# Kernel tuning notes

Hardware: AMD Instinct MI355X
Metric: run time of the kernel (lower is better)

The kernel has to match this reference:

```python
import jax, jax.numpy as jnp
import numpy as np

B, N, M = 8, 4096, 2048
IN_DIM, D, CTX_DIM = 512, 512, 768


def setup_inputs() -> dict:
    key = jax.random.key(0)
    k_h, k_hr, k_c, k_a, k_k, k_v, k_o = jax.random.split(key, 7)
    s = 0.02  # init scale for weights
    return {
        "h": jax.random.normal(k_h, (B, N, IN_DIM), dtype=jnp.float32),
        "h_retrieved": jax.random.normal(k_hr, (B, M, CTX_DIM), dtype=jnp.float32),
        # torch nn.Linear convention: weight is [out_features, in_features]
        "W_cond": jax.random.normal(k_c, (IN_DIM, CTX_DIM), dtype=jnp.float32) * s,
        "W_attn": jax.random.normal(k_a, (D, IN_DIM), dtype=jnp.float32) * s,
        "W_k": jax.random.normal(k_k, (D, IN_DIM), dtype=jnp.float32) * s,
        "W_v": jax.random.normal(k_v, (D, IN_DIM), dtype=jnp.float32) * s,
        "W_out": jax.random.normal(k_o, (IN_DIM, D), dtype=jnp.float32) * s,
    }


def reference(h, h_retrieved, W_cond, W_attn, W_k, W_v, W_out):
    # cond_flag is True since context_dim != in_dim
    hr = h_retrieved @ W_cond.T                      # [B, M, in_dim]
    attn = jax.nn.softmax(h @ W_attn.T, axis=-1)     # [B, N, d], softmax over channel dim
    kv_in = jnp.concatenate([h, hr], axis=1)         # [B, N+M, in_dim]
    k = kv_in @ W_k.T                                # [B, N+M, d]
    v = kv_in @ W_v.T                                # [B, N+M, d]
    f = jnp.einsum('bnd,bne->bde', k, v)             # K^T V: [B, d, d]
    h_aug = jnp.einsum('bnd,bde->bne', attn, f)      # [B, N, d]
    return h + h_aug @ W_out.T                       # [B, N, in_dim]
```

## Files before the change

### kernel.cpp

```cpp
#include <hip/hip_runtime.h>
#include <hip/hip_bf16.h>


typedef unsigned short u16;
typedef __bf16 bf16x8 __attribute__((ext_vector_type(8)));
typedef float  f32x4  __attribute__((ext_vector_type(4)));
typedef float  f32v4  __attribute__((ext_vector_type(4)));
typedef u16    u16v4  __attribute__((ext_vector_type(4)));
typedef u16    u16v8  __attribute__((ext_vector_type(8)));

__device__ __forceinline__ u16 f2bf(float f) {
  unsigned u = __builtin_bit_cast(unsigned, f);
  u = u + 0x7FFFu + ((u >> 16) & 1u);
  return (u16)(u >> 16);
}
__device__ __forceinline__ float bf2f(u16 s) {
  return __builtin_bit_cast(float, (unsigned)s << 16);
}

__global__ __launch_bounds__(256) void cvt_T(const float* __restrict__ src,
                                             u16* __restrict__ dstT,
                                             long src_bs, long dstT_bs) {
  __shared__ u16 tile[64][72];
  long bz = blockIdx.z;
  const float* S = src + bz * src_bs;
  u16* DT = dstT + bz * dstT_bs;
  int r0 = blockIdx.x * 64;
  int c0 = blockIdx.y * 64;
  int t  = threadIdx.x;
  int tr = t >> 2;
  int tc = (t & 3) * 16;
  const float* sp = &S[(long)(r0 + tr) * 512 + c0 + tc];
#pragma unroll
  for (int q = 0; q < 2; ++q) {
    f32v4 a = *(const f32v4*)(sp + q * 8);
    f32v4 b = *(const f32v4*)(sp + q * 8 + 4);
    u16v8 o;
    o[0] = f2bf(a[0]); o[1] = f2bf(a[1]); o[2] = f2bf(a[2]); o[3] = f2bf(a[3]);
    o[4] = f2bf(b[0]); o[5] = f2bf(b[1]); o[6] = f2bf(b[2]); o[7] = f2bf(b[3]);
    *(u16v8*)&tile[tr][tc + q * 8] = o;
  }
  __syncthreads();
  int tr2 = t >> 3;
  int tc2 = (t & 7) * 8;
#pragma unroll
  for (int it = 0; it < 2; ++it) {
    int cr = it * 32 + tr2;
    u16v8 o;
#pragma unroll
    for (int j = 0; j < 8; ++j) o[j] = tile[tc2 + j][cr];
    *(u16v8*)&DT[(long)(c0 + cr) * 6144 + r0 + tc2] = o;
  }
}

__global__ __launch_bounds__(256) void prep_weights(
    const float* __restrict__ Wc, const float* __restrict__ Wa,
    const float* __restrict__ Wk, const float* __restrict__ Wv,
    const float* __restrict__ Wo,
    u16* __restrict__ wc, u16* __restrict__ wa, u16* __restrict__ wk,
    u16* __restrict__ wv, u16* __restrict__ wvT, u16* __restrict__ wo) {
  __shared__ u16 tile[64][72];
  int bx = blockIdx.x;
  int t = threadIdx.x;
  if (bx < 576) {
    const float* src; u16* dst; long base;
    if (bx < 192)      { src = Wc; dst = wc; base = (long)bx * 2048; }
    else if (bx < 320) { src = Wa; dst = wa; base = (long)(bx - 192) * 2048; }
    else if (bx < 448) { src = Wk; dst = wk; base = (long)(bx - 320) * 2048; }
    else               { src = Wo; dst = wo; base = (long)(bx - 448) * 2048; }
    long i = base + (long)t * 8;
    f32v4 a = *(const f32v4*)(src + i);
    f32v4 b = *(const f32v4*)(src + i + 4);
    u16v8 o;
    o[0] = f2bf(a[0]); o[1] = f2bf(a[1]); o[2] = f2bf(a[2]); o[3] = f2bf(a[3]);
    o[4] = f2bf(b[0]); o[5] = f2bf(b[1]); o[6] = f2bf(b[2]); o[7] = f2bf(b[3]);
    *(u16v8*)(dst + i) = o;
  } else {
    int b2 = bx - 576;
    int r0 = (b2 >> 3) * 64, c0 = (b2 & 7) * 64;
    int tr = t >> 2, tc = (t & 3) * 16;
    const float* sp = &Wv[(long)(r0 + tr) * 512 + c0 + tc];
#pragma unroll
    for (int q = 0; q < 2; ++q) {
      f32v4 a = *(const f32v4*)(sp + q * 8);
      f32v4 b = *(const f32v4*)(sp + q * 8 + 4);
      u16v8 o;
      o[0] = f2bf(a[0]); o[1] = f2bf(a[1]); o[2] = f2bf(a[2]); o[3] = f2bf(a[3]);
      o[4] = f2bf(b[0]); o[5] = f2bf(b[1]); o[6] = f2bf(b[2]); o[7] = f2bf(b[3]);
      *(u16v8*)&wv[(long)(r0 + tr) * 512 + c0 + tc + q * 8] = o;
      *(u16v8*)&tile[tr][tc + q * 8] = o;
    }
    __syncthreads();
    int tr2 = t >> 3, tc2 = (t & 7) * 8;
#pragma unroll
    for (int it = 0; it < 2; ++it) {
      int cr = it * 32 + tr2;
      u16v8 o;
#pragma unroll
      for (int j = 0; j < 8; ++j) o[j] = tile[tc2 + j][cr];
      *(u16v8*)&wvT[(long)(c0 + cr) * 512 + r0 + tc2] = o;
    }
  }
}

__global__ __launch_bounds__(256) void reduce8_bf16(const u16* __restrict__ parts,
                                                    u16* __restrict__ out) {
  long i = (((long)blockIdx.x * 256) + threadIdx.x) * 8;
  long b = i >> 18;
  long r = i & 262143;
  const u16* p = parts + b * 2097152 + r;
  float acc[8] = {};
#pragma unroll
  for (int s = 0; s < 8; ++s) {
    u16v8 v = *(const u16v8*)(p + (long)s * 262144);
#pragma unroll
    for (int j = 0; j < 8; ++j) acc[j] += bf2f(v[j]);
  }
  u16v8 o;
#pragma unroll
  for (int j = 0; j < 8; ++j) o[j] = f2bf(acc[j]);
  *(u16v8*)(out + i) = o;
}

template <int MODE, bool AF32>
__global__ __launch_bounds__(256) void gemm_nt(
    const void* __restrict__ Ap, const u16* __restrict__ B, void* __restrict__ Cout,
    const float* __restrict__ Res, int K, int lda, int ldb, int ldc,
    long sA, long sB, long sC, long sS, long sRes, int kslices) {
  __shared__ __align__(16) char smem_c[65536];

  int gx = gridDim.x, gy = gridDim.y;
  int nwg = gx * gy * (int)gridDim.z;
  int flat = blockIdx.x + gx * (blockIdx.y + gy * blockIdx.z);
  if ((nwg & 7) == 0) { int q = nwg >> 3; flat = (flat & 7) * q + (flat >> 3); }
  int bx = flat % gx; int tmp = flat / gx; int by = tmp % gy; int z = tmp / gy;

  int b = z / kslices;
  int s = z - b * kslices;

  int mt = bx, nt = by;
  if constexpr (MODE == 4) {
    if (bx < 4)      { mt = 0; nt = bx; }
    else if (bx < 7) { mt = 1; nt = bx - 3; }
    else if (bx < 9) { mt = 2; nt = bx - 5; }
    else             { mt = 3; nt = 3; }
  }
  long m0 = (long)mt * 128;
  long n0 = (long)nt * 128;

  const u16* Ag = (const u16*)Ap + (long)b * sA + (long)s * K;
  const float* Af = (const float*)Ap + (long)b * sA;
  const u16* Bg = B + (long)b * sB + (long)s * K;

  int tid  = threadIdx.x;
  int lane = tid & 63;
  int wid  = tid >> 6;
  int wm = wid >> 1, wn = wid & 1;

  int srow = wid * 8 + (lane >> 3);
  int scol = (lane & 7) * 8;
  int arow  = tid >> 1;
  int acolb = (tid & 1) * 32;

  auto stageA = [&](u16* Asd, int k0) {
#pragma unroll
    for (int c = 0; c < 4; ++c) {
      int row = c * 32 + srow;
      __builtin_amdgcn_global_load_lds(
          (const __attribute__((address_space(1))) void*)(Ag + (m0 + row) * lda + k0 + scol),
          (__attribute__((address_space(3))) void*)(Asd + (c * 32 + wid * 8) * 64),
          16, 0, 0);
    }
  };
  auto stageB = [&](u16* Bsd, int k0) {
#pragma unroll
    for (int c = 0; c < 4; ++c) {
      int row = c * 32 + srow;
      __builtin_amdgcn_global_load_lds(
          (const __attribute__((address_space(1))) void*)(Bg + (n0 + row) * ldb + k0 + scol),
          (__attribute__((address_space(3))) void*)(Bsd + (c * 32 + wid * 8) * 64),
          16, 0, 0);
    }
  };
  f32v4 xr[8];
  auto loadA = [&](int k0) {
    const float* sp = Af + (m0 + arow) * (long)lda + k0 + acolb;
#pragma unroll
    for (int q = 0; q < 8; ++q) xr[q] = *(const f32v4*)(sp + q * 4);
  };
  auto cvtA = [&](u16* Asd) {
#pragma unroll
    for (int q = 0; q < 4; ++q) {
      u16v8 o;
      o[0] = f2bf(xr[2*q][0]); o[1] = f2bf(xr[2*q][1]);
      o[2] = f2bf(xr[2*q][2]); o[3] = f2bf(xr[2*q][3]);
      o[4] = f2bf(xr[2*q+1][0]); o[5] = f2bf(xr[2*q+1][1]);
      o[6] = f2bf(xr[2*q+1][2]); o[7] = f2bf(xr[2*q+1][3]);
      *(u16v8*)&Asd[arow * 64 + acolb + q * 8] = o;
    }
  };

  f32x4 acc[4][4] = {};
  int nk = K >> 6;

  if constexpr (AF32) {
    loadA(0);
    cvtA((u16*)smem_c);
    asm volatile("s_waitcnt lgkmcnt(0)" ::: "memory");
  } else {
    stageA((u16*)smem_c, 0);
  }
  stageB((u16*)(smem_c + 32768), 0);

  for (int t = 0; t < nk; ++t) {
    u16* Asc = (u16*)(smem_c + (t & 1) * 16384);
    u16* Bsc = (u16*)(smem_c + 32768 + (t & 1) * 16384);
    u16* Asn = (u16*)(smem_c + ((t + 1) & 1) * 16384);
    u16* Bsn = (u16*)(smem_c + 32768 + ((t + 1) & 1) * 16384);
    bool more = (t + 1) < nk;
    if (more) {
      if constexpr (AF32) {
        loadA((t + 1) * 64);
        stageB(Bsn, (t + 1) * 64);
        asm volatile("s_waitcnt vmcnt(12)\n\ts_barrier" ::: "memory");
      } else {
        stageA(Asn, (t + 1) * 64);
        stageB(Bsn, (t + 1) * 64);
        asm volatile("s_waitcnt vmcnt(8)\n\ts_barrier" ::: "memory");
      }
    } else {
      asm volatile("s_waitcnt vmcnt(0)\n\ts_barrier" ::: "memory");
    }
#pragma unroll
    for (int kk = 0; kk < 2; ++kk) {
      int kofs = kk * 32 + (lane >> 4) * 8;
      bf16x8 af[4], bfr[4];
#pragma unroll
      for (int i = 0; i < 4; ++i) {
        af[i]  = *(const bf16x8*)&Asc[(wm * 64 + i * 16 + (lane & 15)) * 64 + kofs];
        bfr[i] = *(const bf16x8*)&Bsc[(wn * 64 + i * 16 + (lane & 15)) * 64 + kofs];
      }
#pragma unroll
      for (int i = 0; i < 4; ++i)
#pragma unroll
        for (int j = 0; j < 4; ++j)
          acc[i][j] = __builtin_amdgcn_mfma_f32_16x16x32_bf16(af[i], bfr[j], acc[i][j], 0, 0, 0);
    }
    if constexpr (AF32) {
      if (more) cvtA(Asn);
      asm volatile("s_waitcnt lgkmcnt(0)\n\ts_barrier" ::: "memory");
    } else {
      asm volatile("s_barrier" ::: "memory");
    }
  }

  long cb = (long)b * sC + (long)s * sS;
  int lq = lane >> 4;
  int lr = lane & 15;

  if constexpr (MODE == 0 || MODE == 1 || MODE == 4) {
    float* ep = (float*)(smem_c + wid * 4608);
    int row0 = (int)m0 + wm * 64;
    int colb = (int)n0 + wn * 64;
#pragma unroll
    for (int i = 0; i < 4; ++i) {
#pragma unroll
      for (int j = 0; j < 4; ++j)
#pragma unroll
        for (int r = 0; r < 4; ++r)
          ep[(lq * 4 + r) * 72 + lr + j * 16] = acc[i][j][r];
#pragma unroll
      for (int p = 0; p < 4; ++p) {
        int rl = p * 4 + lq;
        f32x4 v = *(f32x4*)&ep[rl * 72 + lr * 4];
        long off = (long)(row0 + i * 16 + rl) * ldc + colb + lr * 4;
        if (MODE == 0 || MODE == 4) {
          u16v4 o;
#pragma unroll
          for (int t2 = 0; t2 < 4; ++t2) o[t2] = f2bf(v[t2]);
          *(u16v4*)((u16*)Cout + cb + off) = o;
        } else {
          const float* R = Res + (long)b * sRes;
          f32v4 rv = *(const f32v4*)&R[off];
          f32v4 ov;
#pragma unroll
          for (int t2 = 0; t2 < 4; ++t2) ov[t2] = v[t2] + rv[t2];
          *(f32v4*)((float*)Cout + cb + off) = ov;
        }
      }
    }
    if constexpr (MODE == 4) {
      if (mt != nt) {
        u16* tT = (u16*)(smem_c + 18432);
#pragma unroll
        for (int i = 0; i < 4; ++i)
#pragma unroll
          for (int j = 0; j < 4; ++j)
#pragma unroll
            for (int r = 0; r < 4; ++r)
              tT[(wn * 64 + j * 16 + lr) * 136 + wm * 64 + i * 16 + lq * 4 + r] =
                  f2bf(acc[i][j][r]);
        __syncthreads();
        int ct   = tid >> 1;
        int half = (tid & 1) * 64;
        u16* dst = (u16*)Cout + cb + (long)(n0 + ct) * ldc + m0 + half;
        const u16* srcl = &tT[ct * 136 + half];
#pragma unroll
        for (int q = 0; q < 8; ++q)
          *(u16v8*)(dst + q * 8) = *(const u16v8*)(srcl + q * 8);
      }
    }
  } else {
    u16* tT = (u16*)smem_c;
#pragma unroll
    for (int i = 0; i < 4; ++i)
#pragma unroll
      for (int j = 0; j < 4; ++j)
#pragma unroll
        for (int r = 0; r < 4; ++r)
          tT[(wn * 64 + j * 16 + lr) * 136 + wm * 64 + i * 16 + lq * 4 + r] =
              f2bf(acc[i][j][r]);
    __syncthreads();
    int ct   = tid >> 1;
    int half = (tid & 1) * 64;
    u16* dst = (u16*)Cout + cb + (long)(n0 + ct) * ldc + m0 + half;
    const u16* srcl = &tT[ct * 136 + half];
#pragma unroll
    for (int q = 0; q < 8; ++q)
      *(u16v8*)(dst + q * 8) = *(const u16v8*)(srcl + q * 8);
  }
}

__global__ __launch_bounds__(256) void gemm64(
    const u16* __restrict__ A, const u16* __restrict__ B, u16* __restrict__ Cout,
    int K, int lda, int ldb, int ldc, long sA, long sB, long sC) {
  __shared__ __align__(16) char smem_c[49152];

  int gx = gridDim.x, gy = gridDim.y;
  int nwg = gx * gy * (int)gridDim.z;
  int flat = blockIdx.x + gx * (blockIdx.y + gy * blockIdx.z);
  if ((nwg & 7) == 0) { int q = nwg >> 3; flat = (flat & 7) * q + (flat >> 3); }
  int bx = flat % gx; int tmp = flat / gx; int by = tmp % gy; int b = tmp / gy;

  long n0 = (long)bx * 128;
  long m0 = (long)by * 64;
  const u16* Ag = A + (long)b * sA;
  const u16* Bg = B + (long)b * sB;

  int tid  = threadIdx.x;
  int lane = tid & 63;
  int wid  = tid >> 6;
  int wm = wid >> 1, wn = wid & 1;

  int srow = wid * 8 + (lane >> 3);
  int scol = (lane & 7) * 8;

  auto stageA = [&](u16* Asd, int k0) {
#pragma unroll
    for (int c = 0; c < 2; ++c) {
      int row = c * 32 + srow;
      __builtin_amdgcn_global_load_lds(
          (const __attribute__((address_space(1))) void*)(Ag + (m0 + row) * lda + k0 + scol),
          (__attribute__((address_space(3))) void*)(Asd + (c * 32 + wid * 8) * 64),
          16, 0, 0);
    }
  };
  auto stageB = [&](u16* Bsd, int k0) {
#pragma unroll
    for (int c = 0; c < 4; ++c) {
      int row = c * 32 + srow;
      __builtin_amdgcn_global_load_lds(
          (const __attribute__((address_space(1))) void*)(Bg + (n0 + row) * ldb + k0 + scol),
          (__attribute__((address_space(3))) void*)(Bsd + (c * 32 + wid * 8) * 64),
          16, 0, 0);
    }
  };

  f32x4 acc[2][4] = {};
  int nk = K >> 6;

  stageA((u16*)smem_c, 0);
  stageB((u16*)(smem_c + 16384), 0);

  for (int t = 0; t < nk; ++t) {
    u16* Asc = (u16*)(smem_c + (t & 1) * 8192);
    u16* Bsc = (u16*)(smem_c + 16384 + (t & 1) * 16384);
    u16* Asn = (u16*)(smem_c + ((t + 1) & 1) * 8192);
    u16* Bsn = (u16*)(smem_c + 16384 + ((t + 1) & 1) * 16384);
    bool more = (t + 1) < nk;
    if (more) {
      stageA(Asn, (t + 1) * 64);
      stageB(Bsn, (t + 1) * 64);
      asm volatile("s_waitcnt vmcnt(6)\n\ts_barrier" ::: "memory");
    } else {
      asm volatile("s_waitcnt vmcnt(0)\n\ts_barrier" ::: "memory");
    }
#pragma unroll
    for (int kk = 0; kk < 2; ++kk) {
      int kofs = kk * 32 + (lane >> 4) * 8;
      bf16x8 af[2], bfr[4];
#pragma unroll
      for (int i = 0; i < 2; ++i)
        af[i]  = *(const bf16x8*)&Asc[(wm * 32 + i * 16 + (lane & 15)) * 64 + kofs];
#pragma unroll
      for (int j = 0; j < 4; ++j)
        bfr[j] = *(const bf16x8*)&Bsc[(wn * 64 + j * 16 + (lane & 15)) * 64 + kofs];
#pragma unroll
      for (int i = 0; i < 2; ++i)
#pragma unroll
        for (int j = 0; j < 4; ++j)
          acc[i][j] = __builtin_amdgcn_mfma_f32_16x16x32_bf16(af[i], bfr[j], acc[i][j], 0, 0, 0);
    }
    asm volatile("s_barrier" ::: "memory");
  }

  int lq = lane >> 4;
  int lr = lane & 15;
  float* ep = (float*)(smem_c + wid * 4608);
  long cb  = (long)b * sC;
  int row0 = (int)m0 + wm * 32;
  int colb = (int)n0 + wn * 64;
#pragma unroll
  for (int i = 0; i < 2; ++i) {
#pragma unroll
    for (int j = 0; j < 4; ++j)
#pragma unroll
      for (int r = 0; r < 4; ++r)
        ep[(lq * 4 + r) * 72 + lr + j * 16] = acc[i][j][r];
#pragma unroll
    for (int p = 0; p < 4; ++p) {
      int rl = p * 4 + lq;
      f32x4 v = *(f32x4*)&ep[rl * 72 + lr * 4];
      long off = (long)(row0 + i * 16 + rl) * ldc + colb + lr * 4;
      u16v4 o;
#pragma unroll
      for (int t2 = 0; t2 < 4; ++t2) o[t2] = f2bf(v[t2]);
      *(u16v4*)(Cout + cb + off) = o;
    }
  }
}

__global__ __launch_bounds__(256, 2) void gemm_sm(
    const float* __restrict__ A,
    const u16* __restrict__ Bw,
    u16* __restrict__ C) {
  __shared__ __align__(16) char smem[73728];
  u16* As = (u16*)smem;
  u16* Bs = (u16*)(smem + 8192);

  int nwg = gridDim.x;
  int flat = blockIdx.x;
  if ((nwg & 7) == 0) { int q = nwg >> 3; flat = (flat & 7) * q + (flat >> 3); }
  long m0 = (long)flat * 64;

  int tid = threadIdx.x;
  int lane = tid & 63;
  int wid = tid >> 6;

  int srow = wid * 8 + (lane >> 3);
  int scol = (lane & 7) * 8;
  int arow  = tid >> 2;
  int acolb = (tid & 3) * 16;

  f32x4 acc[4][8] = {};

  for (int k0 = 0; k0 < 512; k0 += 64) {
    const float* sp = A + (m0 + arow) * 512 + k0 + acolb;
    f32v4 x0 = *(const f32v4*)sp;
    f32v4 x1 = *(const f32v4*)(sp + 4);
    f32v4 x2 = *(const f32v4*)(sp + 8);
    f32v4 x3 = *(const f32v4*)(sp + 12);
#pragma unroll
    for (int c = 0; c < 16; ++c) {
      int row = c * 32 + srow;
      __builtin_amdgcn_global_load_lds(
          (const __attribute__((address_space(1))) void*)(Bw + (long)row * 512 + k0 + scol),
          (__attribute__((address_space(3))) void*)(Bs + (c * 32 + wid * 8) * 64),
          16, 0, 0);
    }
    u16v8 o0, o1;
    o0[0] = f2bf(x0[0]); o0[1] = f2bf(x0[1]); o0[2] = f2bf(x0[2]); o0[3] = f2bf(x0[3]);
    o0[4] = f2bf(x1[0]); o0[5] = f2bf(x1[1]); o0[6] = f2bf(x1[2]); o0[7] = f2bf(x1[3]);
    o1[0] = f2bf(x2[0]); o1[1] = f2bf(x2[1]); o1[2] = f2bf(x2[2]); o1[3] = f2bf(x2[3]);
    o1[4] = f2bf(x3[0]); o1[5] = f2bf(x3[1]); o1[6] = f2bf(x3[2]); o1[7] = f2bf(x3[3]);
    *(u16v8*)&As[arow * 64 + acolb] = o0;
    *(u16v8*)&As[arow * 64 + acolb + 8] = o1;
    __syncthreads();
#pragma unroll
    for (int kk = 0; kk < 2; ++kk) {
      int kofs = kk * 32 + (lane >> 4) * 8;
      bf16x8 af[4], bfr[8];
#pragma unroll
      for (int i = 0; i < 4; ++i)
        af[i] = *(const bf16x8*)&As[(i * 16 + (lane & 15)) * 64 + kofs];
#pragma unroll
      for (int j = 0; j < 8; ++j)
        bfr[j] = *(const bf16x8*)&Bs[(wid * 128 + j * 16 + (lane & 15)) * 64 + kofs];
#pragma unroll
      for (int i = 0; i < 4; ++i)
#pragma unroll
        for (int j = 0; j < 8; ++j)
          acc[i][j] = __builtin_amdgcn_mfma_f32_16x16x32_bf16(af[i], bfr[j], acc[i][j], 0, 0, 0);
    }
    __syncthreads();
  }

  int lq = lane >> 4, lr = lane & 15;
  float* sm = (float*)smem;
  float* ss = (float*)(smem + 1024);

#pragma unroll
  for (int i = 0; i < 4; ++i)
#pragma unroll
    for (int r = 0; r < 4; ++r) {
      float m = acc[i][0][r];
#pragma unroll
      for (int j = 1; j < 8; ++j) m = fmaxf(m, acc[i][j][r]);
#pragma unroll
      for (int o = 1; o < 16; o <<= 1) m = fmaxf(m, __shfl_xor(m, o, 16));
      if (lr == 0) sm[(i * 16 + lq * 4 + r) * 4 + wid] = m;
    }
  __syncthreads();
  float rinv[4][4];
#pragma unroll
  for (int i = 0; i < 4; ++i)
#pragma unroll
    for (int r = 0; r < 4; ++r) {
      f32v4 g4 = *(const f32v4*)&sm[(i * 16 + lq * 4 + r) * 4];
      float gm = fmaxf(fmaxf(g4[0], g4[1]), fmaxf(g4[2], g4[3]));
      float s = 0.f;
#pragma unroll
      for (int j = 0; j < 8; ++j) {
        float e = __expf(acc[i][j][r] - gm);
        acc[i][j][r] = e;
        s += e;
      }
#pragma unroll
      for (int o = 1; o < 16; o <<= 1) s += __shfl_xor(s, o, 16);
      if (lr == 0) ss[(i * 16 + lq * 4 + r) * 4 + wid] = s;
    }
  __syncthreads();
#pragma unroll
  for (int i = 0; i < 4; ++i)
#pragma unroll
    for (int r = 0; r < 4; ++r) {
      f32v4 g4 = *(const f32v4*)&ss[(i * 16 + lq * 4 + r) * 4];
      rinv[i][r] = 1.0f / (g4[0] + g4[1] + g4[2] + g4[3]);
    }
  __syncthreads();

  float* ep = (float*)(smem + wid * 4608);
#pragma unroll
  for (int i = 0; i < 4; ++i) {
#pragma unroll
    for (int jh = 0; jh < 2; ++jh) {
#pragma unroll
      for (int j = 0; j < 4; ++j)
#pragma unroll
        for (int r = 0; r < 4; ++r)
          ep[(lq * 4 + r) * 72 + lr + j * 16] = acc[i][jh * 4 + j][r] * rinv[i][r];
#pragma unroll
      for (int p = 0; p < 4; ++p) {
        int rl = p * 4 + lq;
        f32x4 v = *(f32x4*)&ep[rl * 72 + lr * 4];
        u16v4 o;
#pragma unroll
        for (int t = 0; t < 4; ++t) o[t] = f2bf(v[t]);
        *(u16v4*)&C[(m0 + i * 16 + rl) * 512 + wid * 128 + jh * 64 + lr * 4] = o;
      }
    }
  }
}

extern "C" void kernel_launch(void* const* d_in, const int* in_sizes, int n_in,
                              void* d_out, int out_size, void* d_ws, size_t ws_size,
                              hipStream_t stream) {
  (void)in_sizes; (void)n_in; (void)out_size; (void)ws_size;
  const float* h    = (const float*)d_in[0];
  const float* hret = (const float*)d_in[1];
  const float* Wc   = (const float*)d_in[2];
  const float* Wa   = (const float*)d_in[3];
  const float* Wk   = (const float*)d_in[4];
  const float* Wv   = (const float*)d_in[5];
  const float* Wo   = (const float*)d_in[6];
  float* out = (float*)d_out;
  char*  ws  = (char*)d_ws;

  constexpr long MB = 1024 * 1024;
  u16*   w_cond = (u16*)(ws + 0);
  u16*   w_attn = (u16*)(ws + 786432);
  u16*   w_k    = (u16*)(ws + 1310720);
  u16*   w_v    = (u16*)(ws + 1835008);
  u16*   w_out  = (u16*)(ws + 2359296);
  u16*   w_vT   = (u16*)(ws + 2883584);
  u16*   gparts = (u16*)(ws + 4 * MB);
  u16*   attn   = (u16*)(ws + 36 * MB);
  u16*   g_bf   = (u16*)(ws + 68 * MB);
  u16*   u_mat  = (u16*)(ws + 72 * MB);
  u16*   v1     = (u16*)(ws + 73 * MB);
  u16*   f2t    = (u16*)(ws + 77 * MB);
  u16*   xt     = (u16*)(ws + 84 * MB);

  cvt_T<<<dim3(64, 8, 8), 256, 0, stream>>>(h, xt, 2097152L, 3145728L);
  prep_weights<<<640, 256, 0, stream>>>(Wc, Wa, Wk, Wv, Wo,
      w_cond, w_attn, w_k, w_v, w_vT, w_out);

  gemm_nt<3, true><<<dim3(16, 4, 8), 256, 0, stream>>>(hret, w_cond, xt + 4096, nullptr,
      768, 768, 768, 6144, 1572864L, 0, 3145728L, 0, 0, 1);

  gemm_sm<<<512, 256, 0, stream>>>(h, w_attn, attn);

  gemm_nt<4, false><<<dim3(10, 1, 64), 256, 0, stream>>>(xt, xt, gparts, nullptr,
      768, 6144, 6144, 512, 3145728L, 3145728L, 2097152L, 262144L, 0, 8);
  reduce8_bf16<<<1024, 256, 0, stream>>>(gparts, g_bf);

  gemm64<<<dim3(4, 8, 1), 256, 0, stream>>>(w_out, w_vT, u_mat,
      512, 512, 512, 512, 0, 0, 0);
  gemm64<<<dim3(4, 8, 8), 256, 0, stream>>>(u_mat, g_bf, v1,
      512, 512, 512, 512, 0, 262144L, 262144L);
  gemm64<<<dim3(4, 8, 8), 256, 0, stream>>>(v1, w_k, f2t,
      512, 512, 512, 512, 262144L, 0, 262144L);

  gemm_nt<1, false><<<dim3(32, 4, 8), 256, 0, stream>>>(attn, f2t, out, h,
      512, 512, 512, 512, 2097152L, 262144L, 2097152L, 0, 2097152L, 1);
}
```

Before: 210.3 us.

## Add 256x256 tile GEMM with direct-to-LDS loads for Gram and output GEMMs

```diff
diff --git a/kernel.cpp b/kernel.cpp
--- a/kernel.cpp
+++ b/kernel.cpp
@@ -122,6 +122,130 @@
   *(u16v8*)(out + i) = o;
 }
 
+template <int MODE>
+__global__ __launch_bounds__(512, 2) void gemm256(
+    const u16* __restrict__ A, const u16* __restrict__ B, void* __restrict__ Cout,
+    const float* __restrict__ Res, int K, int lda, int ldb, int ldc,
+    long sA, long sB, long sC, long sS, long sRes, int kslices) {
+  __shared__ __align__(16) u16 lds[65536];
+
+  int gx = gridDim.x, gy = gridDim.y;
+  int nwg = gx * gy * (int)gridDim.z;
+  int flat = blockIdx.x + gx * (blockIdx.y + gy * blockIdx.z);
+  if ((nwg & 7) == 0) { int q = nwg >> 3; flat = (flat & 7) * q + (flat >> 3); }
+  int bx = flat % gx; int tmp = flat / gx; int by = tmp % gy; int z = tmp / gy;
+  int b = z / kslices;
+  int s = z - b * kslices;
+
+  long m0 = (long)bx * 256;
+  long n0 = (long)by * 256;
+  const u16* Ag = A + (long)b * sA + (long)s * K;
+  const u16* Bg = B + (long)b * sB + (long)s * K;
+
+  int tid  = threadIdx.x;
+  int lane = tid & 63;
+  int wid  = tid >> 6;
+  int wm = wid >> 2;
+  int wn = wid & 3;
+  int l15 = lane & 15, l16 = lane >> 4, l7 = lane & 7;
+
+  auto stage_half = [&](bool isA, int buf, int h, int ktile) {
+    const u16* G = isA ? Ag : Bg;
+    long rb = (isA ? m0 : n0) + h * 128;
+    int ldg = isA ? lda : ldb;
+    u16* base = lds + (isA ? 0 : 32768) + buf * 16384 + h * 8192;
+    int row_lo = wid * 8 + (lane >> 3);
+    int ce = ((lane & 7) ^ ((lane >> 3) & 7)) * 8;
+#pragma unroll
+    for (int q = 0; q < 2; ++q) {
+      const u16* src = G + (rb + q * 64 + row_lo) * (long)ldg + ktile * 64 + ce;
+      u16* dst = base + (q * 512 + wid * 64) * 8;
+      __builtin_amdgcn_global_load_lds(
+          (const __attribute__((address_space(1))) void*)src,
+          (__attribute__((address_space(3))) void*)dst, 16, 0, 0);
+    }
+  };
+
+  f32x4 acc[8][4] = {};
+  int nk = K >> 6;
+
+  stage_half(true,  0, 0, 0); stage_half(true,  0, 1, 0);
+  stage_half(false, 0, 0, 0); stage_half(false, 0, 1, 0);
+
+  for (int kt = 0; kt < nk; ++kt) {
+    int cur = kt & 1, nxt = cur ^ 1;
+    asm volatile("s_waitcnt vmcnt(0)\n\ts_barrier" ::: "memory");
+    const u16* Ab = lds + cur * 16384 + wm * 8192;
+    const u16* Bb = lds + 32768 + cur * 16384 + (wn >> 1) * 8192 + (wn & 1) * 4096;
+    bool more = (kt + 1) < nk;
+#pragma unroll
+    for (int kk = 0; kk < 2; ++kk) {
+      int csw = ((kk * 4 + l16) ^ l7) * 8;
+      bf16x8 bf[4];
+#pragma unroll
+      for (int j = 0; j < 4; ++j)
+        bf[j] = *(const bf16x8*)&Bb[(j * 16 + l15) * 64 + csw];
+#pragma unroll
+      for (int frh = 0; frh < 2; ++frh) {
+        bf16x8 af[4];
+#pragma unroll
+        for (int i = 0; i < 4; ++i)
+          af[i] = *(const bf16x8*)&Ab[((frh * 4 + i) * 16 + l15) * 64 + csw];
+        if (more) {
+          if (kk == 0 && frh == 0) {
+            stage_half(true, nxt, 0, kt + 1); stage_half(true, nxt, 1, kt + 1);
+          } else if (kk == 0 && frh == 1) {
+            stage_half(false, nxt, 0, kt + 1); stage_half(false, nxt, 1, kt + 1);
+          }
+        }
+        asm volatile("s_barrier" ::: "memory");
+        __builtin_amdgcn_s_setprio(1);
+#pragma unroll
+        for (int i = 0; i < 4; ++i)
+#pragma unroll
+          for (int j = 0; j < 4; ++j)
+            acc[frh * 4 + i][j] = __builtin_amdgcn_mfma_f32_16x16x32_bf16(
+                af[i], bf[j], acc[frh * 4 + i][j], 0, 0, 0);
+        __builtin_amdgcn_s_setprio(0);
+        asm volatile("s_barrier" ::: "memory");
+      }
+    }
+  }
+
+  int lq = l16, lr = l15;
+  float* ep = (float*)((char*)lds + wid * 4608);
+  long cb  = (long)b * sC + (long)s * sS;
+  int row0 = (int)m0 + wm * 128;
+  int colb = (int)n0 + wn * 64;
+#pragma unroll
+  for (int fr = 0; fr < 8; ++fr) {
+#pragma unroll
+    for (int j = 0; j < 4; ++j)
+#pragma unroll
+      for (int r = 0; r < 4; ++r)
+        ep[(lq * 4 + r) * 72 + lr + j * 16] = acc[fr][j][r];
+#pragma unroll
+    for (int p = 0; p < 4; ++p) {
+      int rl = p * 4 + lq;
+      f32x4 v = *(f32x4*)&ep[rl * 72 + lr * 4];
+      long off = (long)(row0 + fr * 16 + rl) * ldc + colb + lr * 4;
+      if (MODE == 0) {
+        u16v4 o;
+#pragma unroll
+        for (int t2 = 0; t2 < 4; ++t2) o[t2] = f2bf(v[t2]);
+        *(u16v4*)((u16*)Cout + cb + off) = o;
+      } else {
+        const float* R = Res + (long)b * sRes;
+        f32v4 rv = *(const f32v4*)&R[off];
+        f32v4 ov;
+#pragma unroll
+        for (int t2 = 0; t2 < 4; ++t2) ov[t2] = v[t2] + rv[t2];
+        *(f32v4*)((float*)Cout + cb + off) = ov;
+      }
+    }
+  }
+}
+
 template <int MODE, bool AF32>
 __global__ __launch_bounds__(256) void gemm_nt(
     const void* __restrict__ Ap, const u16* __restrict__ B, void* __restrict__ Cout,
@@ -138,15 +262,8 @@
   int b = z / kslices;
   int s = z - b * kslices;
 
-  int mt = bx, nt = by;
-  if constexpr (MODE == 4) {
-    if (bx < 4)      { mt = 0; nt = bx; }
-    else if (bx < 7) { mt = 1; nt = bx - 3; }
-    else if (bx < 9) { mt = 2; nt = bx - 5; }
-    else             { mt = 3; nt = 3; }
-  }
-  long m0 = (long)mt * 128;
-  long n0 = (long)nt * 128;
+  long m0 = (long)bx * 128;
+  long n0 = (long)by * 128;
 
   const u16* Ag = (const u16*)Ap + (long)b * sA + (long)s * K;
   const float* Af = (const float*)Ap + (long)b * sA;
@@ -258,59 +375,7 @@
   int lq = lane >> 4;
   int lr = lane & 15;
 
-  if constexpr (MODE == 0 || MODE == 1 || MODE == 4) {
-    float* ep = (float*)(smem_c + wid * 4608);
-    int row0 = (int)m0 + wm * 64;
-    int colb = (int)n0 + wn * 64;
-#pragma unroll
-    for (int i = 0; i < 4; ++i) {
-#pragma unroll
-      for (int j = 0; j < 4; ++j)
-#pragma unroll
-        for (int r = 0; r < 4; ++r)
-          ep[(lq * 4 + r) * 72 + lr + j * 16] = acc[i][j][r];
-#pragma unroll
-      for (int p = 0; p < 4; ++p) {
-        int rl = p * 4 + lq;
-        f32x4 v = *(f32x4*)&ep[rl * 72 + lr * 4];
-        long off = (long)(row0 + i * 16 + rl) * ldc + colb + lr * 4;
-        if (MODE == 0 || MODE == 4) {
-          u16v4 o;
-#pragma unroll
-          for (int t2 = 0; t2 < 4; ++t2) o[t2] = f2bf(v[t2]);
-          *(u16v4*)((u16*)Cout + cb + off) = o;
-        } else {
-          const float* R = Res + (long)b * sRes;
-          f32v4 rv = *(const f32v4*)&R[off];
-          f32v4 ov;
-#pragma unroll
-          for (int t2 = 0; t2 < 4; ++t2) ov[t2] = v[t2] + rv[t2];
-          *(f32v4*)((float*)Cout + cb + off) = ov;
-        }
-      }
-    }
-    if constexpr (MODE == 4) {
-      if (mt != nt) {
-        u16* tT = (u16*)(smem_c + 18432);
-#pragma unroll
-        for (int i = 0; i < 4; ++i)
-#pragma unroll
-          for (int j = 0; j < 4; ++j)
-#pragma unroll
-            for (int r = 0; r < 4; ++r)
-              tT[(wn * 64 + j * 16 + lr) * 136 + wm * 64 + i * 16 + lq * 4 + r] =
-                  f2bf(acc[i][j][r]);
-        __syncthreads();
-        int ct   = tid >> 1;
-        int half = (tid & 1) * 64;
-        u16* dst = (u16*)Cout + cb + (long)(n0 + ct) * ldc + m0 + half;
-        const u16* srcl = &tT[ct * 136 + half];
-#pragma unroll
-        for (int q = 0; q < 8; ++q)
-          *(u16v8*)(dst + q * 8) = *(const u16v8*)(srcl + q * 8);
-      }
-    }
-  } else {
+  if constexpr (MODE == 3) {
     u16* tT = (u16*)smem_c;
 #pragma unroll
     for (int i = 0; i < 4; ++i)
@@ -328,6 +393,28 @@
 #pragma unroll
     for (int q = 0; q < 8; ++q)
       *(u16v8*)(dst + q * 8) = *(const u16v8*)(srcl + q * 8);
+  } else {
+    float* ep = (float*)(smem_c + wid * 4608);
+    int row0 = (int)m0 + wm * 64;
+    int colb = (int)n0 + wn * 64;
+#pragma unroll
+    for (int i = 0; i < 4; ++i) {
+#pragma unroll
+      for (int j = 0; j < 4; ++j)
+#pragma unroll
+        for (int r = 0; r < 4; ++r)
+          ep[(lq * 4 + r) * 72 + lr + j * 16] = acc[i][j][r];
+#pragma unroll
+      for (int p = 0; p < 4; ++p) {
+        int rl = p * 4 + lq;
+        f32x4 v = *(f32x4*)&ep[rl * 72 + lr * 4];
+        long off = (long)(row0 + i * 16 + rl) * ldc + colb + lr * 4;
+        u16v4 o;
+#pragma unroll
+        for (int t2 = 0; t2 < 4; ++t2) o[t2] = f2bf(v[t2]);
+        *(u16v4*)((u16*)Cout + cb + off) = o;
+      }
+    }
   }
 }
 
@@ -610,7 +697,7 @@
 
   gemm_sm<<<512, 256, 0, stream>>>(h, w_attn, attn);
 
-  gemm_nt<4, false><<<dim3(10, 1, 64), 256, 0, stream>>>(xt, xt, gparts, nullptr,
+  gemm256<0><<<dim3(2, 2, 64), 512, 0, stream>>>(xt, xt, gparts, nullptr,
       768, 6144, 6144, 512, 3145728L, 3145728L, 2097152L, 262144L, 0, 8);
   reduce8_bf16<<<1024, 256, 0, stream>>>(gparts, g_bf);
 
@@ -621,6 +708,6 @@
   gemm64<<<dim3(4, 8, 8), 256, 0, stream>>>(v1, w_k, f2t,
       512, 512, 512, 512, 262144L, 0, 262144L);
 
-  gemm_nt<1, false><<<dim3(32, 4, 8), 256, 0, stream>>>(attn, f2t, out, h,
+  gemm256<1><<<dim3(16, 2, 8), 512, 0, stream>>>(attn, f2t, out, h,
       512, 512, 512, 512, 2097152L, 262144L, 2097152L, 0, 2097152L, 1);
 }
```

Result: faster. 200.3 us (-4.7%).

## Triple-buffer gemm_nt pipeline and move hret bf16 conversion to a separate kernel

Applied to the files above, without the earlier changes.

```diff
diff --git a/kernel.cpp b/kernel.cpp
--- a/kernel.cpp
+++ b/kernel.cpp
@@ -16,6 +16,18 @@
 }
 __device__ __forceinline__ float bf2f(u16 s) {
   return __builtin_bit_cast(float, (unsigned)s << 16);
+}
+
+__global__ __launch_bounds__(256) void cvt_f32_bf16(const float* __restrict__ in,
+                                                    u16* __restrict__ out, long n) {
+  long i = (((long)blockIdx.x * 256) + threadIdx.x) * 8;
+  if (i >= n) return;
+  f32v4 a = *(const f32v4*)(in + i);
+  f32v4 b = *(const f32v4*)(in + i + 4);
+  u16v8 o;
+  o[0] = f2bf(a[0]); o[1] = f2bf(a[1]); o[2] = f2bf(a[2]); o[3] = f2bf(a[3]);
+  o[4] = f2bf(b[0]); o[5] = f2bf(b[1]); o[6] = f2bf(b[2]); o[7] = f2bf(b[3]);
+  *(u16v8*)(out + i) = o;
 }
 
 __global__ __launch_bounds__(256) void cvt_T(const float* __restrict__ src,
@@ -122,12 +134,12 @@
   *(u16v8*)(out + i) = o;
 }
 
-template <int MODE, bool AF32>
+template <int MODE>
 __global__ __launch_bounds__(256) void gemm_nt(
-    const void* __restrict__ Ap, const u16* __restrict__ B, void* __restrict__ Cout,
+    const u16* __restrict__ A, const u16* __restrict__ B, void* __restrict__ Cout,
     const float* __restrict__ Res, int K, int lda, int ldb, int ldc,
     long sA, long sB, long sC, long sS, long sRes, int kslices) {
-  __shared__ __align__(16) char smem_c[65536];
+  __shared__ __align__(16) char smem_c[98304];
 
   int gx = gridDim.x, gy = gridDim.y;
   int nwg = gx * gy * (int)gridDim.z;
@@ -137,20 +149,11 @@
 
   int b = z / kslices;
   int s = z - b * kslices;
-
-  int mt = bx, nt = by;
-  if constexpr (MODE == 4) {
-    if (bx < 4)      { mt = 0; nt = bx; }
-    else if (bx < 7) { mt = 1; nt = bx - 3; }
-    else if (bx < 9) { mt = 2; nt = bx - 5; }
-    else             { mt = 3; nt = 3; }
-  }
-  long m0 = (long)mt * 128;
-  long n0 = (long)nt * 128;
-
-  const u16* Ag = (const u16*)Ap + (long)b * sA + (long)s * K;
-  const float* Af = (const float*)Ap + (long)b * sA;
+  const u16* Ag = A + (long)b * sA + (long)s * K;
   const u16* Bg = B + (long)b * sB + (long)s * K;
+
+  long m0 = (long)bx * 128;
+  long n0 = (long)by * 128;
 
   int tid  = threadIdx.x;
   int lane = tid & 63;
@@ -159,10 +162,9 @@
 
   int srow = wid * 8 + (lane >> 3);
   int scol = (lane & 7) * 8;
-  int arow  = tid >> 1;
-  int acolb = (tid & 1) * 32;
-
-  auto stageA = [&](u16* Asd, int k0) {
+
+  auto stageA = [&](int buf, int k0) {
+    u16* Asd = (u16*)(smem_c + buf * 16384);
 #pragma unroll
     for (int c = 0; c < 4; ++c) {
       int row = c * 32 + srow;
@@ -172,7 +174,8 @@
           16, 0, 0);
     }
   };
-  auto stageB = [&](u16* Bsd, int k0) {
+  auto stageB = [&](int buf, int k0) {
+    u16* Bsd = (u16*)(smem_c + 49152 + buf * 16384);
 #pragma unroll
     for (int c = 0; c < 4; ++c) {
       int row = c * 32 + srow;
@@ -182,55 +185,27 @@
           16, 0, 0);
     }
   };
-  f32v4 xr[8];
-  auto loadA = [&](int k0) {
-    const float* sp = Af + (m0 + arow) * (long)lda + k0 + acolb;
-#pragma unroll
-    for (int q = 0; q < 8; ++q) xr[q] = *(const f32v4*)(sp + q * 4);
-  };
-  auto cvtA = [&](u16* Asd) {
-#pragma unroll
-    for (int q = 0; q < 4; ++q) {
-      u16v8 o;
-      o[0] = f2bf(xr[2*q][0]); o[1] = f2bf(xr[2*q][1]);
-      o[2] = f2bf(xr[2*q][2]); o[3] = f2bf(xr[2*q][3]);
-      o[4] = f2bf(xr[2*q+1][0]); o[5] = f2bf(xr[2*q+1][1]);
-      o[6] = f2bf(xr[2*q+1][2]); o[7] = f2bf(xr[2*q+1][3]);
-      *(u16v8*)&Asd[arow * 64 + acolb + q * 8] = o;
-    }
-  };
 
   f32x4 acc[4][4] = {};
   int nk = K >> 6;
 
-  if constexpr (AF32) {
-    loadA(0);
-    cvtA((u16*)smem_c);
-    asm volatile("s_waitcnt lgkmcnt(0)" ::: "memory");
-  } else {
-    stageA((u16*)smem_c, 0);
-  }
-  stageB((u16*)(smem_c + 32768), 0);
-
-  for (int t = 0; t < nk; ++t) {
-    u16* Asc = (u16*)(smem_c + (t & 1) * 16384);
-    u16* Bsc = (u16*)(smem_c + 32768 + (t & 1) * 16384);
-    u16* Asn = (u16*)(smem_c + ((t + 1) & 1) * 16384);
-    u16* Bsn = (u16*)(smem_c + 32768 + ((t + 1) & 1) * 16384);
-    bool more = (t + 1) < nk;
-    if (more) {
-      if constexpr (AF32) {
-        loadA((t + 1) * 64);
-        stageB(Bsn, (t + 1) * 64);
-        asm volatile("s_waitcnt vmcnt(12)\n\ts_barrier" ::: "memory");
-      } else {
-        stageA(Asn, (t + 1) * 64);
-        stageB(Bsn, (t + 1) * 64);
-        asm volatile("s_waitcnt vmcnt(8)\n\ts_barrier" ::: "memory");
-      }
+  stageA(0, 0); stageB(0, 0);
+  if (nk > 1) { stageA(1, 64); stageB(1, 64); }
+
+  int cur = 0;
+  for (int kt = 0; kt < nk; ++kt) {
+    if (kt + 1 < nk) {
+      asm volatile("s_waitcnt vmcnt(8)\n\ts_barrier" ::: "memory");
     } else {
       asm volatile("s_waitcnt vmcnt(0)\n\ts_barrier" ::: "memory");
     }
+    if (kt + 2 < nk) {
+      int tgt = cur + 2; if (tgt >= 3) tgt -= 3;
+      stageA(tgt, (kt + 2) * 64);
+      stageB(tgt, (kt + 2) * 64);
+    }
+    const u16* Asc = (const u16*)(smem_c + cur * 16384);
+    const u16* Bsc = (const u16*)(smem_c + 49152 + cur * 16384);
 #pragma unroll
     for (int kk = 0; kk < 2; ++kk) {
       int kofs = kk * 32 + (lane >> 4) * 8;
@@ -246,88 +221,44 @@
         for (int j = 0; j < 4; ++j)
           acc[i][j] = __builtin_amdgcn_mfma_f32_16x16x32_bf16(af[i], bfr[j], acc[i][j], 0, 0, 0);
     }
-    if constexpr (AF32) {
-      if (more) cvtA(Asn);
-      asm volatile("s_waitcnt lgkmcnt(0)\n\ts_barrier" ::: "memory");
-    } else {
-      asm volatile("s_barrier" ::: "memory");
-    }
-  }
-
-  long cb = (long)b * sC + (long)s * sS;
+    ++cur; if (cur >= 3) cur = 0;
+  }
+
+  __syncthreads();
+
+  float* ep = (float*)(smem_c + wid * 4608);
+  long cb  = (long)b * sC + (long)s * sS;
+  int row0 = (int)m0 + wm * 64;
+  int colb = (int)n0 + wn * 64;
   int lq = lane >> 4;
   int lr = lane & 15;
 
-  if constexpr (MODE == 0 || MODE == 1 || MODE == 4) {
-    float* ep = (float*)(smem_c + wid * 4608);
-    int row0 = (int)m0 + wm * 64;
-    int colb = (int)n0 + wn * 64;
-#pragma unroll
-    for (int i = 0; i < 4; ++i) {
-#pragma unroll
-      for (int j = 0; j < 4; ++j)
-#pragma unroll
-        for (int r = 0; r < 4; ++r)
-          ep[(lq * 4 + r) * 72 + lr + j * 16] = acc[i][j][r];
-#pragma unroll
-      for (int p = 0; p < 4; ++p) {
-        int rl = p * 4 + lq;
-        f32x4 v = *(f32x4*)&ep[rl * 72 + lr * 4];
-        long off = (long)(row0 + i * 16 + rl) * ldc + colb + lr * 4;
-        if (MODE == 0 || MODE == 4) {
-          u16v4 o;
-#pragma unroll
-          for (int t2 = 0; t2 < 4; ++t2) o[t2] = f2bf(v[t2]);
-          *(u16v4*)((u16*)Cout + cb + off) = o;
-        } else {
-          const float* R = Res + (long)b * sRes;
-          f32v4 rv = *(const f32v4*)&R[off];
-          f32v4 ov;
-#pragma unroll
-          for (int t2 = 0; t2 < 4; ++t2) ov[t2] = v[t2] + rv[t2];
-          *(f32v4*)((float*)Cout + cb + off) = ov;
-        }
+#pragma unroll
+  for (int i = 0; i < 4; ++i) {
+#pragma unroll
+    for (int j = 0; j < 4; ++j)
+#pragma unroll
+      for (int r = 0; r < 4; ++r)
+        ep[(lq * 4 + r) * 72 + lr + j * 16] = acc[i][j][r];
+#pragma unroll
+    for (int p = 0; p < 4; ++p) {
+      int rl = p * 4 + lq;
+      f32x4 v = *(f32x4*)&ep[rl * 72 + lr * 4];
+      long off = (long)(row0 + i * 16 + rl) * ldc + colb + lr * 4;
+      if (MODE == 0) {
+        u16v4 o;
+#pragma unroll
+        for (int t2 = 0; t2 < 4; ++t2) o[t2] = f2bf(v[t2]);
+        *(u16v4*)((u16*)Cout + cb + off) = o;
+      } else {
+        const float* R = Res + (long)b * sRes;
+        f32v4 rv = *(const f32v4*)&R[off];
+        f32v4 ov;
+#pragma unroll
+        for (int t2 = 0; t2 < 4; ++t2) ov[t2] = v[t2] + rv[t2];
+        *(f32v4*)((float*)Cout + cb + off) = ov;
       }
     }
-    if constexpr (MODE == 4) {
-      if (mt != nt) {
-        u16* tT = (u16*)(smem_c + 18432);
-#pragma unroll
-        for (int i = 0; i < 4; ++i)
-#pragma unroll
-          for (int j = 0; j < 4; ++j)
-#pragma unroll
-            for (int r = 0; r < 4; ++r)
-              tT[(wn * 64 + j * 16 + lr) * 136 + wm * 64 + i * 16 + lq * 4 + r] =
-                  f2bf(acc[i][j][r]);
-        __syncthreads();
-        int ct   = tid >> 1;
-        int half = (tid & 1) * 64;
-        u16* dst = (u16*)Cout + cb + (long)(n0 + ct) * ldc + m0 + half;
-        const u16* srcl = &tT[ct * 136 + half];
-#pragma unroll
-        for (int q = 0; q < 8; ++q)
-          *(u16v8*)(dst + q * 8) = *(const u16v8*)(srcl + q * 8);
-      }
-    }
-  } else {
-    u16* tT = (u16*)smem_c;
-#pragma unroll
-    for (int i = 0; i < 4; ++i)
-#pragma unroll
-      for (int j = 0; j < 4; ++j)
-#pragma unroll
-        for (int r = 0; r < 4; ++r)
-          tT[(wn * 64 + j * 16 + lr) * 136 + wm * 64 + i * 16 + lq * 4 + r] =
-              f2bf(acc[i][j][r]);
-    __syncthreads();
-    int ct   = tid >> 1;
-    int half = (tid & 1) * 64;
-    u16* dst = (u16*)Cout + cb + (long)(n0 + ct) * ldc + m0 + half;
-    const u16* srcl = &tT[ct * 136 + half];
-#pragma unroll
-    for (int q = 0; q < 8; ++q)
-      *(u16v8*)(dst + q * 8) = *(const u16v8*)(srcl + q * 8);
   }
 }
 
@@ -587,30 +518,32 @@
   char*  ws  = (char*)d_ws;
 
   constexpr long MB = 1024 * 1024;
-  u16*   w_cond = (u16*)(ws + 0);
-  u16*   w_attn = (u16*)(ws + 786432);
-  u16*   w_k    = (u16*)(ws + 1310720);
-  u16*   w_v    = (u16*)(ws + 1835008);
-  u16*   w_out  = (u16*)(ws + 2359296);
-  u16*   w_vT   = (u16*)(ws + 2883584);
-  u16*   gparts = (u16*)(ws + 4 * MB);
-  u16*   attn   = (u16*)(ws + 36 * MB);
-  u16*   g_bf   = (u16*)(ws + 68 * MB);
-  u16*   u_mat  = (u16*)(ws + 72 * MB);
-  u16*   v1     = (u16*)(ws + 73 * MB);
-  u16*   f2t    = (u16*)(ws + 77 * MB);
-  u16*   xt     = (u16*)(ws + 84 * MB);
+  u16*   w_cond  = (u16*)(ws + 0);
+  u16*   w_attn  = (u16*)(ws + 786432);
+  u16*   w_k     = (u16*)(ws + 1310720);
+  u16*   w_v     = (u16*)(ws + 1835008);
+  u16*   w_out   = (u16*)(ws + 2359296);
+  u16*   w_vT    = (u16*)(ws + 2883584);
+  u16*   hret_bf = (u16*)(ws + 4 * MB);
+  u16*   gparts  = (u16*)(ws + 4 * MB);
+  u16*   attn    = (u16*)(ws + 36 * MB);
+  u16*   g_bf    = (u16*)(ws + 68 * MB);
+  u16*   u_mat   = (u16*)(ws + 72 * MB);
+  u16*   v1      = (u16*)(ws + 73 * MB);
+  u16*   f2t     = (u16*)(ws + 77 * MB);
+  u16*   xt      = (u16*)(ws + 84 * MB);
 
   cvt_T<<<dim3(64, 8, 8), 256, 0, stream>>>(h, xt, 2097152L, 3145728L);
   prep_weights<<<640, 256, 0, stream>>>(Wc, Wa, Wk, Wv, Wo,
       w_cond, w_attn, w_k, w_v, w_vT, w_out);
-
-  gemm_nt<3, true><<<dim3(16, 4, 8), 256, 0, stream>>>(hret, w_cond, xt + 4096, nullptr,
-      768, 768, 768, 6144, 1572864L, 0, 3145728L, 0, 0, 1);
+  cvt_f32_bf16<<<6144, 256, 0, stream>>>(hret, hret_bf, 12582912L);
+
+  gemm_nt<0><<<dim3(4, 16, 8), 256, 0, stream>>>(w_cond, hret_bf, xt + 4096, nullptr,
+      768, 768, 768, 6144, 0, 1572864L, 3145728L, 0, 0, 1);
 
   gemm_sm<<<512, 256, 0, stream>>>(h, w_attn, attn);
 
-  gemm_nt<4, false><<<dim3(10, 1, 64), 256, 0, stream>>>(xt, xt, gparts, nullptr,
+  gemm_nt<0><<<dim3(4, 4, 64), 256, 0, stream>>>(xt, xt, gparts, nullptr,
       768, 6144, 6144, 512, 3145728L, 3145728L, 2097152L, 262144L, 0, 8);
   reduce8_bf16<<<1024, 256, 0, stream>>>(gparts, g_bf);
 
@@ -621,6 +554,6 @@
   gemm64<<<dim3(4, 8, 8), 256, 0, stream>>>(v1, w_k, f2t,
       512, 512, 512, 512, 262144L, 0, 262144L);
 
-  gemm_nt<1, false><<<dim3(32, 4, 8), 256, 0, stream>>>(attn, f2t, out, h,
+  gemm_nt<1><<<dim3(32, 4, 8), 256, 0, stream>>>(attn, f2t, out, h,
       512, 512, 512, 512, 2097152L, 262144L, 2097152L, 0, 2097152L, 1);
 }
```

Result: slower. 238.3 us (+13.3%).
